# Kernel tuning notes

Hardware: AMD Instinct MI355X
Metric: run time of the kernel (lower is better)

## Reference

```python
import jax, jax.numpy as jnp
import numpy as np

SCALE_FLOOR = 0.001
N_SOURCES = 16


def setup_inputs() -> dict:
    key = jax.random.key(0)
    ks = jax.random.split(key, 8)
    n, d_in, d = 131072, 1024, 512
    x = jax.random.normal(ks[0], (n, d_in), dtype=jnp.float32)
    source_ids = jax.random.randint(ks[1], (n,), 0, N_SOURCES, dtype=jnp.int64)
    # backbone: single Linear(d_in -> d)
    Wb = jax.random.normal(ks[2], (d_in, d), dtype=jnp.float32) / np.sqrt(d_in)
    bb = jax.random.normal(ks[3], (d,), dtype=jnp.float32) * 0.01
    # pooled head: Linear(d -> 2)
    Wp = jax.random.normal(ks[4], (d, 2), dtype=jnp.float32) / np.sqrt(d)
    bp = jax.random.normal(ks[5], (2,), dtype=jnp.float32) * 0.01
    # per-source heads stacked: [S, d, 2], [S, 2]
    Ws = jax.random.normal(ks[6], (N_SOURCES, d, 2), dtype=jnp.float32) / np.sqrt(d)
    bs = jax.random.normal(ks[7], (N_SOURCES, 2), dtype=jnp.float32) * 0.01
    return {"x": x, "source_ids": source_ids, "Wb": Wb, "bb": bb,
            "Wp": Wp, "bp": bp, "Ws": Ws, "bs": bs}


def _head(raw):
    # raw: (n, 2) -> (mu, scale) with softplus + floor on scale
    mu = raw[:, 0]
    scale = jax.nn.softplus(raw[:, 1]) + SCALE_FLOOR
    return mu, scale


def reference(x, source_ids, Wb, bb, Wp, bp, Ws, bs):
    # backbone embedding: (n, d)
    emb = x @ Wb + bb
    # pooled head
    pooled_mu, pooled_scale = _head(emb @ Wp + bp)
    # routed per-source heads: compute all tiny heads, then gather per row.
    # raw_all: (n, S, 2); S*2 is tiny so this beats gather of per-row weights.
    raw_all = jnp.einsum('nd,sdk->nsk', emb, Ws) + bs[None, :, :]
    raw_sel = jnp.take_along_axis(raw_all, source_ids[:, None, None], axis=1)[:, 0, :]
    src_mu, src_scale = _head(raw_sel)
    # all source ids fall in [0, N_SOURCES), so every row is covered
    # (matches the torch loop where unmatched rows would stay zero).
    return emb, pooled_mu, pooled_scale, src_mu, src_scale
```

## Files before the change

kernel.cpp:

```cpp
#include <hip/hip_runtime.h>

typedef short bf16x8 __attribute__((ext_vector_type(8)));
typedef float f32x4 __attribute__((ext_vector_type(4)));

#define NROWS 131072L
#define DIN 1024
#define DEMB 512

__device__ __forceinline__ unsigned short f2bf(float f) {
  unsigned u = __float_as_uint(f);
  u += 0x7FFFu + ((u >> 16) & 1u);
  return (unsigned short)(u >> 16);
}

__device__ __forceinline__ unsigned pkhi(float a, float b) {
  unsigned ua = __float_as_uint(a) + 0x8000u;
  unsigned ub = __float_as_uint(b) + 0x8000u;
  return __builtin_amdgcn_perm(ub, ua, 0x07060302u);
}

__device__ __forceinline__ float softplusf(float v) {
  return fmaxf(v, 0.f) + log1pf(expf(-fabsf(v)));
}

__global__ __launch_bounds__(256) void wb_transpose(const float* __restrict__ Wb,
                                                    unsigned short* __restrict__ WbT) {
  int g = blockIdx.x * 256 + threadIdx.x;
  int n = g & 511;
  int kb = g >> 9;
  unsigned short tmp[8];
#pragma unroll
  for (int j = 0; j < 8; ++j)
    tmp[j] = f2bf(Wb[(kb * 8 + j) * DEMB + n]);
  uint4 v;
  v.x = (unsigned)tmp[0] | ((unsigned)tmp[1] << 16);
  v.y = (unsigned)tmp[2] | ((unsigned)tmp[3] << 16);
  v.z = (unsigned)tmp[4] | ((unsigned)tmp[5] << 16);
  v.w = (unsigned)tmp[6] | ((unsigned)tmp[7] << 16);
  *(uint4*)(WbT + (long)n * DIN + kb * 8) = v;
}

__global__ __launch_bounds__(256, 3) void gemm_bias(const float* __restrict__ x,
                                                    const unsigned short* __restrict__ wbt,
                                                    const float* __restrict__ bb,
                                                    float* __restrict__ emb) {
  __shared__ unsigned short As[2][128 * 32];
  __shared__ unsigned short Bsh[2][128 * 32];

  const int t = threadIdx.x;
  const int lane = t & 63;
  const int wid = t >> 6;
  const int wm = wid >> 1, wn = wid & 1;

  const int bid = blockIdx.x;
  const int swz = (bid & 7) * 512 + (bid >> 3);
  const int ntile = swz & 3;
  const long mtile = swz >> 2;
  const long m0 = mtile * 128;
  const int n0 = ntile * 128;

  const int arow = t >> 3;
  const int akc = t & 7;
  const int abyte = arow * 64 + ((((akc >> 1) ^ ((t >> 4) & 3)) << 4)) + (akc & 1) * 8;
  const float* xbase = x + (m0 + arow) * DIN + akc * 4;

  const int bn = wid * 16 + (lane >> 2);
  const int bsg = (lane & 3) ^ ((lane >> 3) & 3);
  const unsigned short* bsrc = wbt + (long)(n0 + bn) * DIN + bsg * 8;

  const int l15 = lane & 15, lg = lane >> 4;
  const int kgo = ((lg ^ ((l15 >> 1) & 3)) << 4);
  const int ardrow = (wm * 64 + l15) * 64;
  const int brdrow = (wn * 64 + l15) * 64;

  f32x4 acc[4][4] = {};
  float4 areg[4];

  auto loadA = [&](int k0) {
#pragma unroll
    for (int p = 0; p < 4; ++p)
      areg[p] = *(const float4*)(xbase + (long)p * 32 * DIN + k0);
  };
  auto stageB = [&](int b, int k0) {
#pragma unroll
    for (int i = 0; i < 2; ++i) {
      const unsigned short* gp = bsrc + (long)i * 64 * DIN + k0;
      unsigned short* lp = &Bsh[b][(i * 256 + wid * 64) * 8];
      __builtin_amdgcn_global_load_lds(
          (const __attribute__((address_space(1))) void*)gp,
          (__attribute__((address_space(3))) void*)lp, 16, 0, 0);
    }
  };
  auto writeA = [&](int b) {
    char* base = (char*)As[b];
#pragma unroll
    for (int p = 0; p < 4; ++p) {
      uint2 v;
      v.x = pkhi(areg[p].x, areg[p].y);
      v.y = pkhi(areg[p].z, areg[p].w);
      *(uint2*)(base + abyte + p * 2048) = v;
    }
  };
  auto compute = [&](int b) {
    const char* Ab = (const char*)As[b];
    const char* Bb = (const char*)Bsh[b];
    bf16x8 af[4], bf_[4];
#pragma unroll
    for (int i = 0; i < 4; ++i) {
      af[i] = *(const bf16x8*)(Ab + ardrow + i * 1024 + kgo);
      bf_[i] = *(const bf16x8*)(Bb + brdrow + i * 1024 + kgo);
    }
#pragma unroll
    for (int mi = 0; mi < 4; ++mi)
#pragma unroll
      for (int ni = 0; ni < 4; ++ni)
        acc[mi][ni] = __builtin_amdgcn_mfma_f32_16x16x32_bf16(af[mi], bf_[ni],
                                                             acc[mi][ni], 0, 0, 0);
  };

  loadA(0);
  stageB(0, 0);
  writeA(0);
  __syncthreads();

  int buf = 0;
#pragma unroll 1
  for (int tt = 0; tt < 32; ++tt) {
    if (tt + 1 < 32) {
      loadA((tt + 1) * 32);
      stageB(buf ^ 1, (tt + 1) * 32);
    }
    compute(buf);
    if (tt + 1 < 32) writeA(buf ^ 1);
    __syncthreads();
    buf ^= 1;
  }

  const int colg = n0 + wn * 64 + l15;
  float bbv[4];
#pragma unroll
  for (int ni = 0; ni < 4; ++ni) bbv[ni] = bb[colg + ni * 16];
#pragma unroll
  for (int mi = 0; mi < 4; ++mi) {
    const long rbase = m0 + wm * 64 + mi * 16 + lg * 4;
#pragma unroll
    for (int ni = 0; ni < 4; ++ni) {
#pragma unroll
      for (int r = 0; r < 4; ++r)
        emb[(rbase + r) * DEMB + colg + ni * 16] = acc[mi][ni][r] + bbv[ni];
    }
  }
}

__global__ __launch_bounds__(256) void head_kernel(const float* __restrict__ emb,
                                                   const int* __restrict__ sid,
                                                   const float* __restrict__ Wp,
                                                   const float* __restrict__ bp,
                                                   const float* __restrict__ Ws,
                                                   const float* __restrict__ bs,
                                                   float* __restrict__ out) {
  const int t = threadIdx.x;
  const int lane = t & 63;
  const int w = t >> 6;
  const long row = (long)blockIdx.x * 4 + w;
  const float* e = emb + row * DEMB;
  const int s = sid[row];
  const float2* wp2 = (const float2*)Wp;
  const float2* ws2 = (const float2*)(Ws + (long)s * (DEMB * 2));
  float a0 = 0.f, a1 = 0.f, a2 = 0.f, a3 = 0.f;
#pragma unroll
  for (int j = 0; j < 8; ++j) {
    int c = j * 64 + lane;
    float ev = e[c];
    float2 wp = wp2[c];
    float2 wv = ws2[c];
    a0 = fmaf(ev, wp.x, a0);
    a1 = fmaf(ev, wp.y, a1);
    a2 = fmaf(ev, wv.x, a2);
    a3 = fmaf(ev, wv.y, a3);
  }
#pragma unroll
  for (int m = 32; m >= 1; m >>= 1) {
    a0 += __shfl_xor(a0, m);
    a1 += __shfl_xor(a1, m);
    a2 += __shfl_xor(a2, m);
    a3 += __shfl_xor(a3, m);
  }
  if (lane == 0) {
    float* hp = out + NROWS * DEMB;
    hp[row]             = a0 + bp[0];
    hp[NROWS + row]     = softplusf(a1 + bp[1]) + 0.001f;
    hp[2 * NROWS + row] = a2 + bs[s * 2 + 0];
    hp[3 * NROWS + row] = softplusf(a3 + bs[s * 2 + 1]) + 0.001f;
  }
}

extern "C" void kernel_launch(void* const* d_in, const int* in_sizes, int n_in,
                              void* d_out, int out_size, void* d_ws, size_t ws_size,
                              hipStream_t stream) {
  const float* x  = (const float*)d_in[0];
  const int* sid  = (const int*)d_in[1];
  const float* Wb = (const float*)d_in[2];
  const float* bb = (const float*)d_in[3];
  const float* Wp = (const float*)d_in[4];
  const float* bp = (const float*)d_in[5];
  const float* Ws = (const float*)d_in[6];
  const float* bs = (const float*)d_in[7];
  float* out = (float*)d_out;
  unsigned short* WbT = (unsigned short*)d_ws;

  wb_transpose<<<256, 256, 0, stream>>>(Wb, WbT);
  gemm_bias<<<4096, 256, 0, stream>>>(x, WbT, bb, out);
  head_kernel<<<32768, 256, 0, stream>>>(out, sid, Wp, bp, Ws, bs, out);
}
```

Before: 363.9 us.

## Fold head weights into backbone GEMM as extra N tile, drop head kernel

Precomputes Wb·Wp and Wb·Ws (plus folded biases) as 34 extra bf16 weight columns and adds a fifth N tile to the GEMM, so the pooled and per-source head outputs are computed inside the GEMM epilogue with the softplus and source selection done via shared memory. This removes the separate head kernel that reread the full embedding tensor. The GEMM main loop is also rewritten with an explicit two-stage unrolled pipeline and manual waitcnt/barriers. In exchange, the GEMM does an extra mostly-padded tile per row block, which adds MFMA work and rereads x, and the head values now come from bf16-rounded folded weights.

Measured after the change: 360.5 us. About the same (-0.9%).

```diff
diff --git a/kernel.cpp b/kernel.cpp
--- a/kernel.cpp
+++ b/kernel.cpp
@@ -6,6 +6,7 @@
 #define NROWS 131072L
 #define DIN 1024
 #define DEMB 512
+#define NEXT 640
 
 __device__ __forceinline__ unsigned short f2bf(float f) {
   unsigned u = __float_as_uint(f);
@@ -40,12 +41,49 @@
   *(uint4*)(WbT + (long)n * DIN + kb * 8) = v;
 }
 
-__global__ __launch_bounds__(256, 3) void gemm_bias(const float* __restrict__ x,
-                                                    const unsigned short* __restrict__ wbt,
-                                                    const float* __restrict__ bb,
-                                                    float* __restrict__ emb) {
-  __shared__ unsigned short As[2][128 * 32];
-  __shared__ unsigned short Bsh[2][128 * 32];
+__global__ void zero_tail(unsigned* __restrict__ p) {
+  p[blockIdx.x * 256 + threadIdx.x] = 0u;
+}
+
+__global__ __launch_bounds__(256) void wfold_rows(const float* __restrict__ Wb,
+                                                  const float* __restrict__ Wp,
+                                                  const float* __restrict__ Ws,
+                                                  unsigned short* __restrict__ WbT) {
+  int w = threadIdx.x >> 6, lane = threadIdx.x & 63;
+  int k = blockIdx.x * 4 + w;
+  if (lane >= 34) return;
+  const float* src;
+  if (lane < 2) src = Wp + lane;
+  else { int s = (lane - 2) >> 1; src = Ws + s * 1024 + (lane & 1); }
+  const float* wrow = Wb + (long)k * DEMB;
+  float acc = 0.f;
+#pragma unroll 8
+  for (int d = 0; d < DEMB; ++d) acc = fmaf(wrow[d], src[2 * d], acc);
+  WbT[(long)(512 + lane) * DIN + k] = f2bf(acc);
+}
+
+__global__ void bfold_k(const float* __restrict__ bb, const float* __restrict__ Wp,
+                        const float* __restrict__ bp, const float* __restrict__ Ws,
+                        const float* __restrict__ bs, float* __restrict__ bf) {
+  int j = threadIdx.x;
+  if (j >= 34) return;
+  const float* src; float bias;
+  if (j < 2) { src = Wp + j; bias = bp[j]; }
+  else { int s = (j - 2) >> 1; src = Ws + s * 1024 + (j & 1); bias = bs[s * 2 + (j & 1)]; }
+  float acc = bias;
+  for (int d = 0; d < DEMB; ++d) acc = fmaf(bb[d], src[2 * d], acc);
+  bf[j] = acc;
+}
+
+__global__ __launch_bounds__(256, 3) void gemm_fused(
+    const float* __restrict__ x, const unsigned short* __restrict__ wbt,
+    const float* __restrict__ bb, const int* __restrict__ sid,
+    const float* __restrict__ bfold, float* __restrict__ out) {
+  __shared__ unsigned short SM[16384];
+  unsigned short* const As0 = SM;
+  unsigned short* const As1 = SM + 4096;
+  unsigned short* const Bs0 = SM + 8192;
+  unsigned short* const Bs1 = SM + 12288;
 
   const int t = threadIdx.x;
   const int lane = t & 63;
@@ -53,10 +91,10 @@
   const int wm = wid >> 1, wn = wid & 1;
 
   const int bid = blockIdx.x;
-  const int swz = (bid & 7) * 512 + (bid >> 3);
-  const int ntile = swz & 3;
-  const long mtile = swz >> 2;
-  const long m0 = mtile * 128;
+  const int swz = (bid & 7) * 640 + (bid >> 3);
+  const int mtile = swz / 5;
+  const int ntile = swz - mtile * 5;
+  const long m0 = (long)mtile * 128;
   const int n0 = ntile * 128;
 
   const int arow = t >> 3;
@@ -74,124 +112,144 @@
   const int brdrow = (wn * 64 + l15) * 64;
 
   f32x4 acc[4][4] = {};
-  float4 areg[4];
-
-  auto loadA = [&](int k0) {
+  float4 aregA[4], aregB[4];
+
+  auto loadA_A = [&](int k0) {
 #pragma unroll
     for (int p = 0; p < 4; ++p)
-      areg[p] = *(const float4*)(xbase + (long)p * 32 * DIN + k0);
-  };
-  auto stageB = [&](int b, int k0) {
+      aregA[p] = *(const float4*)(xbase + (long)p * 32 * DIN + k0);
+  };
+  auto loadA_B = [&](int k0) {
+#pragma unroll
+    for (int p = 0; p < 4; ++p)
+      aregB[p] = *(const float4*)(xbase + (long)p * 32 * DIN + k0);
+  };
+  auto stageB = [&](unsigned short* dst, int k0) {
 #pragma unroll
     for (int i = 0; i < 2; ++i) {
       const unsigned short* gp = bsrc + (long)i * 64 * DIN + k0;
-      unsigned short* lp = &Bsh[b][(i * 256 + wid * 64) * 8];
+      unsigned short* lp = dst + (i * 256 + wid * 64) * 8;
       __builtin_amdgcn_global_load_lds(
           (const __attribute__((address_space(1))) void*)gp,
           (__attribute__((address_space(3))) void*)lp, 16, 0, 0);
     }
   };
-  auto writeA = [&](int b) {
-    char* base = (char*)As[b];
+  auto writeA_0A = [&]() {
+    char* base = (char*)As0;
 #pragma unroll
     for (int p = 0; p < 4; ++p) {
-      uint2 v;
-      v.x = pkhi(areg[p].x, areg[p].y);
-      v.y = pkhi(areg[p].z, areg[p].w);
+      uint2 v; v.x = pkhi(aregA[p].x, aregA[p].y); v.y = pkhi(aregA[p].z, aregA[p].w);
       *(uint2*)(base + abyte + p * 2048) = v;
     }
   };
-  auto compute = [&](int b) {
-    const char* Ab = (const char*)As[b];
-    const char* Bb = (const char*)Bsh[b];
-    bf16x8 af[4], bf_[4];
+  auto writeA_1B = [&]() {
+    char* base = (char*)As1;
+#pragma unroll
+    for (int p = 0; p < 4; ++p) {
+      uint2 v; v.x = pkhi(aregB[p].x, aregB[p].y); v.y = pkhi(aregB[p].z, aregB[p].w);
+      *(uint2*)(base + abyte + p * 2048) = v;
+    }
+  };
+  auto compute = [&](const unsigned short* Au, const unsigned short* Bu) {
+    const char* Ab = (const char*)Au;
+    const char* Bb = (const char*)Bu;
+    bf16x8 af[4], bfv[4];
 #pragma unroll
     for (int i = 0; i < 4; ++i) {
       af[i] = *(const bf16x8*)(Ab + ardrow + i * 1024 + kgo);
-      bf_[i] = *(const bf16x8*)(Bb + brdrow + i * 1024 + kgo);
+      bfv[i] = *(const bf16x8*)(Bb + brdrow + i * 1024 + kgo);
     }
 #pragma unroll
     for (int mi = 0; mi < 4; ++mi)
 #pragma unroll
       for (int ni = 0; ni < 4; ++ni)
-        acc[mi][ni] = __builtin_amdgcn_mfma_f32_16x16x32_bf16(af[mi], bf_[ni],
+        acc[mi][ni] = __builtin_amdgcn_mfma_f32_16x16x32_bf16(af[mi], bfv[ni],
                                                              acc[mi][ni], 0, 0, 0);
   };
 
-  loadA(0);
-  stageB(0, 0);
-  writeA(0);
-  __syncthreads();
-
-  int buf = 0;
+  stageB(Bs0, 0);
+  loadA_A(0);
+  writeA_0A();
+  loadA_B(32);
+  __builtin_amdgcn_sched_barrier(0);
+  asm volatile("s_waitcnt vmcnt(4) lgkmcnt(0)" ::: "memory");
+  __builtin_amdgcn_sched_barrier(0);
+  __builtin_amdgcn_s_barrier();
+
 #pragma unroll 1
-  for (int tt = 0; tt < 32; ++tt) {
-    if (tt + 1 < 32) {
-      loadA((tt + 1) * 32);
-      stageB(buf ^ 1, (tt + 1) * 32);
-    }
-    compute(buf);
-    if (tt + 1 < 32) writeA(buf ^ 1);
+  for (int it = 0; it < 15; ++it) {
+    const int ke = it * 2;
+    stageB(Bs1, (ke + 1) * 32);
+    __builtin_amdgcn_sched_barrier(0);
+    loadA_A((ke + 2) * 32);
+    compute(As0, Bs0);
+    writeA_1B();
+    __builtin_amdgcn_sched_barrier(0);
+    asm volatile("s_waitcnt vmcnt(4) lgkmcnt(0)" ::: "memory");
+    __builtin_amdgcn_sched_barrier(0);
+    __builtin_amdgcn_s_barrier();
+    stageB(Bs0, (ke + 2) * 32);
+    __builtin_amdgcn_sched_barrier(0);
+    loadA_B((ke + 3) * 32);
+    compute(As1, Bs1);
+    writeA_0A();
+    __builtin_amdgcn_sched_barrier(0);
+    asm volatile("s_waitcnt vmcnt(4) lgkmcnt(0)" ::: "memory");
+    __builtin_amdgcn_sched_barrier(0);
+    __builtin_amdgcn_s_barrier();
+  }
+
+  stageB(Bs1, 31 * 32);
+  compute(As0, Bs0);
+  writeA_1B();
+  __builtin_amdgcn_sched_barrier(0);
+  asm volatile("s_waitcnt vmcnt(0) lgkmcnt(0)" ::: "memory");
+  __builtin_amdgcn_sched_barrier(0);
+  __builtin_amdgcn_s_barrier();
+  compute(As1, Bs1);
+
+  if (ntile < 4) {
+    const int colg = n0 + wn * 64 + l15;
+    float bbv[4];
+#pragma unroll
+    for (int ni = 0; ni < 4; ++ni) bbv[ni] = bb[colg + ni * 16];
+#pragma unroll
+    for (int mi = 0; mi < 4; ++mi) {
+      const long rbase = m0 + wm * 64 + mi * 16 + lg * 4;
+#pragma unroll
+      for (int ni = 0; ni < 4; ++ni)
+#pragma unroll
+        for (int r = 0; r < 4; ++r)
+          out[(rbase + r) * DEMB + colg + ni * 16] = acc[mi][ni][r] + bbv[ni];
+    }
+  } else {
     __syncthreads();
-    buf ^= 1;
-  }
-
-  const int colg = n0 + wn * 64 + l15;
-  float bbv[4];
-#pragma unroll
-  for (int ni = 0; ni < 4; ++ni) bbv[ni] = bb[colg + ni * 16];
-#pragma unroll
-  for (int mi = 0; mi < 4; ++mi) {
-    const long rbase = m0 + wm * 64 + mi * 16 + lg * 4;
-#pragma unroll
-    for (int ni = 0; ni < 4; ++ni) {
-#pragma unroll
-      for (int r = 0; r < 4; ++r)
-        emb[(rbase + r) * DEMB + colg + ni * 16] = acc[mi][ni][r] + bbv[ni];
-    }
-  }
-}
-
-__global__ __launch_bounds__(256) void head_kernel(const float* __restrict__ emb,
-                                                   const int* __restrict__ sid,
-                                                   const float* __restrict__ Wp,
-                                                   const float* __restrict__ bp,
-                                                   const float* __restrict__ Ws,
-                                                   const float* __restrict__ bs,
-                                                   float* __restrict__ out) {
-  const int t = threadIdx.x;
-  const int lane = t & 63;
-  const int w = t >> 6;
-  const long row = (long)blockIdx.x * 4 + w;
-  const float* e = emb + row * DEMB;
-  const int s = sid[row];
-  const float2* wp2 = (const float2*)Wp;
-  const float2* ws2 = (const float2*)(Ws + (long)s * (DEMB * 2));
-  float a0 = 0.f, a1 = 0.f, a2 = 0.f, a3 = 0.f;
-#pragma unroll
-  for (int j = 0; j < 8; ++j) {
-    int c = j * 64 + lane;
-    float ev = e[c];
-    float2 wp = wp2[c];
-    float2 wv = ws2[c];
-    a0 = fmaf(ev, wp.x, a0);
-    a1 = fmaf(ev, wp.y, a1);
-    a2 = fmaf(ev, wv.x, a2);
-    a3 = fmaf(ev, wv.y, a3);
-  }
-#pragma unroll
-  for (int m = 32; m >= 1; m >>= 1) {
-    a0 += __shfl_xor(a0, m);
-    a1 += __shfl_xor(a1, m);
-    a2 += __shfl_xor(a2, m);
-    a3 += __shfl_xor(a3, m);
-  }
-  if (lane == 0) {
-    float* hp = out + NROWS * DEMB;
-    hp[row]             = a0 + bp[0];
-    hp[NROWS + row]     = softplusf(a1 + bp[1]) + 0.001f;
-    hp[2 * NROWS + row] = a2 + bs[s * 2 + 0];
-    hp[3 * NROWS + row] = softplusf(a3 + bs[s * 2 + 1]) + 0.001f;
+    float* hl = (float*)SM;
+    if (wn == 0) {
+#pragma unroll
+      for (int ni = 0; ni < 3; ++ni)
+#pragma unroll
+        for (int mi = 0; mi < 4; ++mi)
+#pragma unroll
+          for (int r = 0; r < 4; ++r) {
+            int row = wm * 64 + mi * 16 + lg * 4 + r;
+            hl[row * 49 + l15 + ni * 16] = acc[mi][ni][r];
+          }
+    }
+    __syncthreads();
+    if (t < 128) {
+      const long row = m0 + t;
+      const int s = sid[row];
+      const float v0 = hl[t * 49 + 0] + bfold[0];
+      const float v1 = hl[t * 49 + 1] + bfold[1];
+      const float v2 = hl[t * 49 + 2 + 2 * s] + bfold[2 + 2 * s];
+      const float v3 = hl[t * 49 + 3 + 2 * s] + bfold[3 + 2 * s];
+      float* hp = out + NROWS * DEMB;
+      hp[row] = v0;
+      hp[NROWS + row] = softplusf(v1) + 0.001f;
+      hp[2 * NROWS + row] = v2;
+      hp[3 * NROWS + row] = softplusf(v3) + 0.001f;
+    }
   }
 }
 
@@ -208,8 +266,11 @@
   const float* bs = (const float*)d_in[7];
   float* out = (float*)d_out;
   unsigned short* WbT = (unsigned short*)d_ws;
+  float* bfoldp = (float*)(WbT + (long)NEXT * DIN);
 
   wb_transpose<<<256, 256, 0, stream>>>(Wb, WbT);
-  gemm_bias<<<4096, 256, 0, stream>>>(x, WbT, bb, out);
-  head_kernel<<<32768, 256, 0, stream>>>(out, sid, Wp, bp, Ws, bs, out);
-}
+  zero_tail<<<188, 256, 0, stream>>>((unsigned*)(WbT + 546 * DIN));
+  wfold_rows<<<256, 256, 0, stream>>>(Wb, Wp, Ws, WbT);
+  bfold_k<<<1, 64, 0, stream>>>(bb, Wp, bp, Ws, bs, bfoldp);
+  gemm_fused<<<5120, 256, 0, stream>>>(x, WbT, bb, sid, bfoldp, out);
+}
```
